# Kernel tuning notes

Hardware: AMD Instinct MI355X
Metric: run time of the kernel (lower is better)

The kernel has to match this reference:

```python
import jax, jax.numpy as jnp
import numpy as np

D_MODEL, N_STATE, L_MAX, BATCH = 256, 64, 4096, 8


def _hippo_pql(n):
    """NPLR-HiPPO decomposition: returns (lambda, p, q) in the eigenbasis (complex)."""
    i = np.arange(1, n + 1, dtype=np.float64)
    hippo = np.where(
        i[:, None] > i[None, :],
        np.sqrt(2 * i[:, None] + 1) * np.sqrt(2 * i[None, :] + 1),
        np.where(i[:, None] == i[None, :], i[:, None] + 1.0, 0.0),
    )
    p = 0.5 * np.sqrt(2 * i + 1.0)
    q = 2 * p
    S = -hippo + p[:, None] * q[None, :]  # normal matrix
    lam, V = np.linalg.eig(S)
    Vc = V.conj().T
    pc = Vc @ p.astype(np.complex128)
    qc = Vc @ q.astype(np.complex128)
    return lam.astype(np.complex64), pc.astype(np.complex64), qc.astype(np.complex64)


def setup_inputs() -> dict:
    key = jax.random.key(0)
    ks = jax.random.split(key, 6)
    lam, p, q = _hippo_pql(N_STATE)
    c2r = lambda z: jnp.asarray(np.stack([z.real, z.imag], axis=-1).astype(np.float32))
    xav = (2.0 / (D_MODEL + N_STATE)) ** 0.5  # xavier-normal std for [D, N]
    log_lo, log_hi = np.log(0.001), np.log(0.1)
    return {
        "u": jax.random.normal(ks[0], (BATCH, L_MAX, D_MODEL), jnp.float32),
        "B_ri": jax.random.normal(ks[1], (D_MODEL, N_STATE, 2), jnp.float32) * xav,
        "Ct_ri": jax.random.normal(ks[2], (D_MODEL, N_STATE, 2), jnp.float32) * xav,
        "lam_ri": c2r(lam),
        "p_ri": c2r(p),
        "q_ri": c2r(q),
        "log_step": jax.random.uniform(ks[3], (D_MODEL,), jnp.float32) * (log_hi - log_lo) + log_lo,
        "D_skip": jnp.ones((D_MODEL,), jnp.float32),
        "W": jax.random.normal(ks[4], (D_MODEL, D_MODEL), jnp.float32) / np.sqrt(D_MODEL),
        "b": jnp.zeros((D_MODEL,), jnp.float32),
        "gamma": jnp.ones((D_MODEL,), jnp.float32),
        "beta": jnp.zeros((D_MODEL,), jnp.float32),
    }


def _c(x):  # [..., 2] real -> complex
    return jax.lax.complex(x[..., 0], x[..., 1])


def _s4_kernel(lam_ri, p_ri, q_ri, B_ri, Ct_ri, log_step, L):
    """DPLR generating-function kernel (annotated-S4 / S4Torch math). Returns K [D, L]."""
    lam, p, q = _c(lam_ri), _c(p_ri), _c(q_ri)  # [N]
    B, Ct = _c(B_ri), _c(Ct_ri)                 # [D, N]
    step = jnp.exp(log_step)                    # [D]
    omega = jnp.exp(-2j * jnp.pi * jnp.arange(L) / L).astype(jnp.complex64)  # [L]
    g = (2.0 / step)[:, None] * ((1.0 - omega) / (1.0 + omega))[None, :]     # [D, L]
    c = 2.0 / (1.0 + omega)                                                  # [L]
    # shared Cauchy resolvent, computed once: [D, L, N]
    r = 1.0 / (g[:, :, None] - lam[None, None, :])
    k00 = jnp.einsum('dn,dln->dl', Ct.conj() * B, r)
    k01 = jnp.einsum('dn,dln->dl', Ct.conj() * p[None, :], r)
    k10 = jnp.einsum('dn,dln->dl', q.conj()[None, :] * B, r)
    k11 = jnp.einsum('n,dln->dl', q.conj() * p, r)
    at_roots = c[None, :] * (k00 - k01 * (1.0 / (1.0 + k11)) * k10)  # [D, L]
    return jnp.fft.ifft(at_roots, n=L, axis=-1).real                  # [D, L]


def reference(u, B_ri, Ct_ri, lam_ri, p_ri, q_ri, log_step, D_skip, W, b, gamma, beta):
    Bsz, L, Dm = u.shape
    K = _s4_kernel(lam_ri, p_ri, q_ri, B_ri, Ct_ri, log_step, L)  # [D, L]
    # non-circular convolution via length-2L FFT
    ud = jnp.fft.rfft(u, n=2 * L, axis=1)        # [B, L+1, D]
    Kd = jnp.fft.rfft(K, n=2 * L, axis=-1)       # [D, L+1]
    conv = jnp.fft.irfft(ud * Kd.T[None], n=2 * L, axis=1)[:, :L, :]
    z = conv + D_skip * u                        # S4Layer output
    z = jax.nn.gelu(z, approximate=False)        # nn.GELU (exact erf)
    z = z @ W.T + b                              # Linear(d, d); dropout p=0 -> identity
    x = z + u                                    # residual
    mu = x.mean(-1, keepdims=True)
    var = x.var(-1, keepdims=True)
    return gamma * (x - mu) * jax.lax.rsqrt(var + 1e-5) + beta  # LayerNorm
```

## Files before the change

### kernel.cpp

```cpp
#include <hip/hip_runtime.h>
#include <math.h>


typedef __attribute__((ext_vector_type(2))) float cf;
typedef __attribute__((ext_vector_type(8))) short bf16x8;
typedef __attribute__((ext_vector_type(4))) float f32x4;

__device__ __forceinline__ cf mkcf(float x, float y){ cf r; r.x = x; r.y = y; return r; }

__device__ __forceinline__ cf cadd(cf a, cf b){ return a + b; }
__device__ __forceinline__ cf csub(cf a, cf b){ return a - b; }
__device__ __forceinline__ cf cscale(cf a, float s){ return a * s; }
__device__ __forceinline__ cf cconj(cf a){ return mkcf(a.x, -a.y); }
__device__ __forceinline__ cf cmul(cf a, cf b){
  return mkcf(fmaf(a.x, b.x, -a.y*b.y), fmaf(a.x, b.y, a.y*b.x));
}
__device__ __forceinline__ void cmacc(cf& acc, cf a, cf b){
  acc.x = fmaf(a.x, b.x, fmaf(-a.y, b.y, acc.x));
  acc.y = fmaf(a.x, b.y, fmaf( a.y, b.x, acc.y));
}
__device__ __forceinline__ cf caddi(cf p, cf q){ return mkcf(p.x - q.y, p.y + q.x); }
__device__ __forceinline__ cf csubi(cf p, cf q){ return mkcf(p.x + q.y, p.y - q.x); }

__device__ __forceinline__ short f2bf(float x){
  union { float f; unsigned u; } v; v.f = x;
  unsigned r = v.u + 0x7fffu + ((v.u >> 16) & 1u);
  return (short)(r >> 16);
}

__device__ __forceinline__ constexpr int RI(int k){ return ((k & 3) << 2) | (k >> 2); }

#define C8 0.92387953251f
#define S8 0.38268343236f
#define RH 0.70710678119f

template<int DIR>
__device__ __forceinline__ void r4(cf& a, cf& b, cf& c, cf& d){
  cf T0 = a + c, T1 = a - c;
  cf T2 = b + d, Bd = b - d;
  a = T0 + T2; c = T0 - T2;
  if (DIR > 0){ b = caddi(T1, Bd); d = csubi(T1, Bd); }
  else        { b = csubi(T1, Bd); d = caddi(T1, Bd); }
}

template<int DIR, bool HZ>
__device__ __forceinline__ void fft16(cf* v){
  if constexpr (HZ){
    #pragma unroll
    for (int i = 0; i < 4; ++i){
      cf a = v[i], b = v[i+4];
      v[i]   = a + b;
      v[i+8] = a - b;
      if (DIR > 0){ v[i+4] = caddi(a, b); v[i+12] = csubi(a, b); }
      else        { v[i+4] = csubi(a, b); v[i+12] = caddi(a, b); }
    }
  } else {
    r4<DIR>(v[0], v[4], v[8],  v[12]);
    r4<DIR>(v[1], v[5], v[9],  v[13]);
    r4<DIR>(v[2], v[6], v[10], v[14]);
    r4<DIR>(v[3], v[7], v[11], v[15]);
  }
  constexpr float D = (float)DIR;
  const cf w1 = mkcf(C8,  D*S8);
  const cf w2 = mkcf(RH,  D*RH);
  const cf w3 = mkcf(S8,  D*C8);
  const cf w6 = mkcf(-RH, D*RH);
  const cf w9 = mkcf(-C8, -D*S8);
  v[5]  = cmul(v[5],  w1);
  v[6]  = cmul(v[6],  w2);
  v[7]  = cmul(v[7],  w3);
  v[9]  = cmul(v[9],  w2);
  v[10] = (DIR > 0) ? mkcf(-v[10].y, v[10].x) : mkcf(v[10].y, -v[10].x);
  v[11] = cmul(v[11], w6);
  v[13] = cmul(v[13], w3);
  v[14] = cmul(v[14], w6);
  v[15] = cmul(v[15], w9);
  r4<DIR>(v[0],  v[1],  v[2],  v[3]);
  r4<DIR>(v[4],  v[5],  v[6],  v[7]);
  r4<DIR>(v[8],  v[9],  v[10], v[11]);
  r4<DIR>(v[12], v[13], v[14], v[15]);
}

template<int DIR, bool HZ = false>
__device__ void fft4096_reg(cf* v, cf* lds){
  const int t = threadIdx.x;
  const int k1 = t >> 4, m2 = t & 15;
  const int swt = t ^ k1;
  constexpr float D = (float)DIR;
  fft16<DIR, HZ>(v);
  float sn, cs;
  __sincosf(D * 1.5339807878856412e-3f * (float)t, &sn, &cs);
  __syncthreads();
  {
    cf* p = lds + swt;
    cf w1 = mkcf(cs, sn);
    p[0]    = v[0];
    p[256]  = cmul(v[RI(1)],  w1);
    cf w2 = cmul(w1, w1);
    p[512]  = cmul(v[RI(2)],  w2);
    cf w3 = cmul(w2, w1);
    p[768]  = cmul(v[RI(3)],  w3);
    cf w4 = cmul(w2, w2);
    p[1024] = cmul(v[RI(4)],  w4);
    cf w5 = cmul(w4, w1);
    p[1280] = cmul(v[RI(5)],  w5);
    cf w6 = cmul(w4, w2);
    p[1536] = cmul(v[RI(6)],  w6);
    cf w7 = cmul(w4, w3);
    p[1792] = cmul(v[RI(7)],  w7);
    cf w8 = cmul(w4, w4);
    p[2048] = cmul(v[RI(8)],  w8);
    p[2304] = cmul(v[RI(9)],  cmul(w8, w1));
    p[2560] = cmul(v[RI(10)], cmul(w8, w2));
    p[2816] = cmul(v[RI(11)], cmul(w8, w3));
    p[3072] = cmul(v[RI(12)], cmul(w8, w4));
    p[3328] = cmul(v[RI(13)], cmul(w8, w5));
    p[3584] = cmul(v[RI(14)], cmul(w8, w6));
    p[3840] = cmul(v[RI(15)], cmul(w8, w7));
  }
  __syncthreads();
  {
    cf* p = lds + k1*256;
    #pragma unroll
    for (int m1 = 0; m1 < 16; ++m1) v[m1] = p[m1*16 + (m2 ^ m1)];
  }
  fft16<DIR, false>(v);
  __sincosf(D * 2.45436926061703e-2f * (float)m2, &sn, &cs);
  __syncthreads();
  {
    cf* p = lds + k1*256;
    cf w1 = mkcf(cs, sn);
    p[m2]              = v[0];
    p[16  + (m2^1)]    = cmul(v[RI(1)],  w1);
    cf w2 = cmul(w1, w1);
    p[32  + (m2^2)]    = cmul(v[RI(2)],  w2);
    cf w3 = cmul(w2, w1);
    p[48  + (m2^3)]    = cmul(v[RI(3)],  w3);
    cf w4 = cmul(w2, w2);
    p[64  + (m2^4)]    = cmul(v[RI(4)],  w4);
    cf w5 = cmul(w4, w1);
    p[80  + (m2^5)]    = cmul(v[RI(5)],  w5);
    cf w6 = cmul(w4, w2);
    p[96  + (m2^6)]    = cmul(v[RI(6)],  w6);
    cf w7 = cmul(w4, w3);
    p[112 + (m2^7)]    = cmul(v[RI(7)],  w7);
    cf w8 = cmul(w4, w4);
    p[128 + (m2^8)]    = cmul(v[RI(8)],  w8);
    p[144 + (m2^9)]    = cmul(v[RI(9)],  cmul(w8, w1));
    p[160 + (m2^10)]   = cmul(v[RI(10)], cmul(w8, w2));
    p[176 + (m2^11)]   = cmul(v[RI(11)], cmul(w8, w3));
    p[192 + (m2^12)]   = cmul(v[RI(12)], cmul(w8, w4));
    p[208 + (m2^13)]   = cmul(v[RI(13)], cmul(w8, w5));
    p[224 + (m2^14)]   = cmul(v[RI(14)], cmul(w8, w6));
    p[240 + (m2^15)]   = cmul(v[RI(15)], cmul(w8, w7));
  }
  __syncthreads();
  {
    const int ka = m2;
    cf* p = lds + k1*256 + ka*16;
    #pragma unroll
    for (int m2b = 0; m2b < 16; ++m2b) v[m2b] = p[m2b ^ ka];
  }
  fft16<DIR, false>(v);
}

__global__ __launch_bounds__(256)
void fused_head(const float* __restrict__ B_ri, const float* __restrict__ Ct_ri,
                const float* __restrict__ lam_ri, const float* __restrict__ p_ri,
                const float* __restrict__ q_ri, const float* __restrict__ log_step,
                float* __restrict__ KdE,
                const float* __restrict__ W, short* __restrict__ Wbf){
  __shared__ cf w00[64], w01[64], w10[64], w11[64], lamS[64];
  const int bid = blockIdx.x;
  const int tid = threadIdx.x;

  if (bid >= 2048){
    int t  = (bid - 2048) * 256 + tid;
    int o4 = t * 4;
    int j   = o4 & 7;
    int lm  = (o4 >> 3)  & 15;
    int lk  = (o4 >> 7)  & 3;
    int nt  = (o4 >> 9)  & 7;
    int fh2 = (o4 >> 12) & 1;
    int ks  = o4 >> 13;
    int f = fh2*128 + nt*16 + lm;
    int k = ks*32 + lk*8 + j;
    float4 wv = *(const float4*)(W + (size_t)f*256 + k);
    short4 o;
    o.x = f2bf(wv.x); o.y = f2bf(wv.y); o.z = f2bf(wv.z); o.w = f2bf(wv.w);
    *(short4*)(Wbf + o4) = o;
    return;
  }

  const int d     = bid >> 3;
  const int chunk = bid & 7;
  const float step = expf(log_step[d]);

  if (tid < 64){
    int n = tid;
    cf Bv = mkcf(B_ri[(d*64+n)*2],  B_ri[(d*64+n)*2+1]);
    cf Cv = mkcf(Ct_ri[(d*64+n)*2], Ct_ri[(d*64+n)*2+1]);
    cf pv = mkcf(p_ri[n*2], p_ri[n*2+1]);
    cf qv = mkcf(q_ri[n*2], q_ri[n*2+1]);
    lamS[n] = mkcf(lam_ri[n*2], lam_ri[n*2+1]);
    cf Cc = cconj(Cv), qc = cconj(qv);
    w00[n] = cmul(Cc, Bv);
    w01[n] = cmul(Cc, pv);
    w10[n] = cmul(qc, Bv);
    w11[n] = cmul(qc, pv);
  }
  __syncthreads();

  cf* out = (cf*)KdE + (size_t)d * 2049;
  const int l = chunk * 256 + tid;
  {
    float th = -(6.28318530717958647692f * (float)l) * (1.0f/4096.0f);
    float sn, cs; __sincosf(th, &sn, &cs);
    cf opw = mkcf(1.0f + cs,  sn);
    cf omw = mkcf(1.0f - cs, -sn);
    float idn = __builtin_amdgcn_rcpf(fmaf(opw.x, opw.x, opw.y*opw.y));
    cf ratio = mkcf((omw.x*opw.x + omw.y*opw.y)*idn,
                    (omw.y*opw.x - omw.x*opw.y)*idn);
    cf g  = cscale(ratio, 2.0f / step);
    cf cc = mkcf(2.0f*opw.x*idn, -2.0f*opw.y*idn);
    cf k00 = mkcf(0,0), k01 = mkcf(0,0), k10 = mkcf(0,0), k11 = mkcf(0,0);
    #pragma unroll 4
    for (int n = 0; n < 64; ++n){
      cf den = g - lamS[n];
      float is = __builtin_amdgcn_rcpf(fmaf(den.x, den.x, den.y*den.y));
      cf r = mkcf(den.x*is, -den.y*is);
      cmacc(k00, w00[n], r);
      cmacc(k01, w01[n], r);
      cmacc(k10, w10[n], r);
      cmacc(k11, w11[n], r);
    }
    cf onep = mkcf(1.0f + k11.x, k11.y);
    float ii = __builtin_amdgcn_rcpf(fmaf(onep.x, onep.x, onep.y*onep.y));
    cf inv1p = mkcf(onep.x*ii, -onep.y*ii);
    cf corr = cmul(k01, cmul(k10, inv1p));
    out[l] = cmul(cc, csub(k00, corr));
  }
  if (chunk == 7 && tid == 255){
    cf s00 = mkcf(0.f, 0.f);
    for (int n = 0; n < 64; ++n) s00 = cadd(s00, w00[n]);
    out[2048] = cscale(s00, 0.5f * step);
  }
}

__device__ void fft_kd_body(int d, cf* L, const float* __restrict__ KdE,
                            float* __restrict__ KdO){
  const int t = threadIdx.x;
  const cf* kdE = (const cf*)KdE + (size_t)d * 2049;
  cf* kdO = (cf*)KdO + (size_t)d * 2048;
  cf v[16];
  const float inv = 1.0f / 4096.0f;
  #pragma unroll
  for (int n1 = 0; n1 < 16; ++n1){
    int m = n1*256 + t;
    cf a = (m <= 2048) ? kdE[m] : cconj(kdE[4096 - m]);
    v[n1] = cscale(a, inv);
  }
  fft4096_reg<+1>(v, L);
  const int k1 = t >> 4, ka = t & 15;
  const int xb = (k1 ^ ka) + 16*ka;
  const int swt = t ^ k1;
  __syncthreads();
  #pragma unroll
  for (int kb = 0; kb < 16; ++kb){
    int g = k1 + 16*ka + 256*kb;
    float kr = v[RI(kb)].x;
    float sn, cs; __sincosf(-7.669903939428206e-4f * (float)g, &sn, &cs);
    L[xb + 256*kb] = mkcf(kr*cs, kr*sn);
  }
  __syncthreads();
  #pragma unroll
  for (int n1 = 0; n1 < 16; ++n1) v[n1] = L[swt + n1*256];
  fft4096_reg<-1>(v, L);
  #pragma unroll
  for (int kb = 0; kb < 8; ++kb)
    kdO[k1 + 16*ka + 256*kb] = v[RI(kb)];
}

__global__ __launch_bounds__(256)
void fused_mid(const float* __restrict__ KdE, float* __restrict__ KdO,
               const float* __restrict__ u, float* __restrict__ ut){
  __shared__ cf L[4096];
  const int bid = blockIdx.x;
  if (bid < 256){
    fft_kd_body(bid, L, KdE, KdO);
    return;
  }
  float (*tile)[33] = (float(*)[33])L;
  const int m  = bid - 256;
  const int l0 = (m & 127) * 32;
  const int d0 = ((m >> 7) & 7) * 32;
  const int b  = m >> 10;
  const int tx = threadIdx.x & 31;
  const int ty = threadIdx.x >> 5;
  const float* ub = u + (size_t)b * 4096 * 256;
  #pragma unroll
  for (int it = 0; it < 4; ++it){
    int l = l0 + ty + it*8;
    tile[tx][ty + it*8] = ub[(size_t)l*256 + d0 + tx];
  }
  __syncthreads();
  float* utb = ut + (size_t)b * 256 * 4096;
  #pragma unroll
  for (int it = 0; it < 4; ++it){
    int dd = d0 + ty + it*8;
    utb[(size_t)dd*4096 + l0 + tx] = tile[ty + it*8][tx];
  }
}

__device__ __forceinline__ float gelu_exact(float x){
  float z = fabsf(x) * 0.70710678118654752f;
  float tt = __builtin_amdgcn_rcpf(fmaf(0.3275911f, z, 1.0f));
  float poly = fmaf(fmaf(fmaf(fmaf(1.061405429f, tt, -1.453152027f), tt,
                    1.421413741f), tt, -0.284496736f), tt, 0.254829592f) * tt;
  float ec = poly * __expf(-z*z);
  float phi = (x >= 0.f) ? fmaf(-0.5f, ec, 1.0f) : 0.5f * ec;
  return x * phi;
}

__global__ __launch_bounds__(256)
void s4_conv(float* __restrict__ ut, const float* __restrict__ KdE,
             const float* __restrict__ KdO, const float* __restrict__ Dsk){
  __shared__ cf L[4096];
  const int row = blockIdx.x;
  const int d   = row & 255;
  const int t   = threadIdx.x;
  cf* rp = (cf*)(ut + (size_t)row * 4096);
  const float dskd = Dsk[d];

  cf v[16], uin[8];
  #pragma unroll
  for (int n1 = 0; n1 < 8; ++n1){ uin[n1] = rp[n1*256 + t]; v[n1] = uin[n1]; }
  #pragma unroll
  for (int n1 = 8; n1 < 16; ++n1) v[n1] = mkcf(0.f, 0.f);

  fft4096_reg<-1, true>(v, L);
  const int k1 = t >> 4, ka = t & 15;
  const int xb  = (k1 ^ ka) + 16*ka;
  const int swt = t ^ k1;
  const int t2  = 256 - t;
  const int swt2 = t2 ^ ((t2 >> 4) & 15);
  __syncthreads();
  #pragma unroll
  for (int kb = 0; kb < 16; ++kb)
    L[xb + 256*kb] = v[RI(kb)];
  __syncthreads();

  const cf* kdE = (const cf*)KdE + (size_t)d * 2049;
  const cf* kdO = (const cf*)KdO + (size_t)d * 2048;
  #pragma unroll
  for (int m = 0; m < 8; ++m){
    int k = t + m*256;
    if (k == 0){
      cf z0 = L[0];
      float U0 = z0.x + z0.y, UN = z0.x - z0.y;
      cf P0 = cscale(kdE[0], U0);
      cf PN = cscale(kdE[2048], UN);
      cf cPN = cconj(PN);
      cf Ep = cscale(cadd(P0, cPN), 0.5f);
      cf Op = cscale(csub(P0, cPN), 0.5f);
      L[0] = mkcf(Ep.x - Op.y, Ep.y + Op.x);
      cf P = cmul(cconj(L[2048]), kdE[1024]);
      L[2048] = cconj(P);
    } else {
      cf zk = L[swt + m*256];
      cf zj = L[(15 - m)*256 + swt2];
      int h = k >> 1;
      cf kk, kj;
      if (k & 1){ kk = kdO[h]; kj = kdO[2047 - h]; }
      else      { kk = kdE[h]; kj = kdE[2048 - h]; }
      float sn, cs; __sincosf(7.669903939428206e-4f * (float)k, &sn, &cs);
      cf KS = mkcf(0.5f*(kk.x + kj.x), 0.5f*(kk.y - kj.y));
      cf KD = mkcf(0.5f*(kk.x - kj.x), 0.5f*(kk.y + kj.y));
      cf KA  = KS - KD * sn;
      cf KAp = KS + KD * sn;
      cf KB  = mkcf(-cs * KD.y, cs * KD.x);
      cf Ak, Aj;
      Ak.x = fmaf(KA.x, zk.x, fmaf(-KA.y, zk.y, fmaf(KB.x, zj.x,  KB.y*zj.y)));
      Ak.y = fmaf(KA.x, zk.y, fmaf( KA.y, zk.x, fmaf(KB.y, zj.x, -KB.x*zj.y)));
      Aj.x = fmaf( KAp.x, zj.x, fmaf(KAp.y, zj.y, fmaf(-KB.x, zk.x, KB.y*zk.y)));
      Aj.y = fmaf(-KAp.y, zj.x, fmaf(KAp.x, zj.y, fmaf( KB.x, zk.y, KB.y*zk.x)));
      L[swt + m*256] = Ak;
      L[(15 - m)*256 + swt2] = Aj;
    }
  }
  __syncthreads();

  #pragma unroll
  for (int n1 = 0; n1 < 16; ++n1) v[n1] = L[swt + n1*256];
  fft4096_reg<+1>(v, L);

  __syncthreads();
  #pragma unroll
  for (int kb = 0; kb < 8; ++kb)
    L[xb + 256*kb] = v[RI(kb)];
  __syncthreads();
  const float inv = 1.0f / 4096.0f;
  unsigned* og = (unsigned*)rp;
  #pragma unroll
  for (int n1 = 0; n1 < 8; ++n1){
    cf cv = L[swt + n1*256];
    float x0 = fmaf(dskd, uin[n1].x, cv.x * inv);
    float x1 = fmaf(dskd, uin[n1].y, cv.y * inv);
    unsigned b0 = (unsigned)(unsigned short)f2bf(gelu_exact(x0));
    unsigned b1 = (unsigned)(unsigned short)f2bf(gelu_exact(x1));
    og[n1*256 + t] = b0 | (b1 << 16);
  }
}

__global__ __launch_bounds__(256)
void mfma_gemm_ln(const float* __restrict__ utg, const short* __restrict__ Wbf,
                  const float* __restrict__ bias, const float* __restrict__ u,
                  const float* __restrict__ gamma, const float* __restrict__ beta,
                  float* __restrict__ out){
  __shared__ short St[64][32];
  __shared__ float prm[2][256];
  __shared__ float2 red[2][2][16];
  const int w    = threadIdx.x >> 6;
  const int l    = threadIdx.x & 63;
  const int lm   = l & 15;
  const int lk   = l >> 4;
  const int tokB = blockIdx.x * 32;
  const int b    = tokB >> 12;
  const int l0   = tokB & 4095;

  prm[0][threadIdx.x] = gamma[threadIdx.x];
  prm[1][threadIdx.x] = beta[threadIdx.x];

  const int srow = l >> 2;
  const int tg   = l & 3;
  const char* ubase = (const char*)utg + (size_t)(b * 256) * 16384;
  bf16x8 pre[4];
  #pragma unroll
  for (int c = 0; c < 4; ++c){
    int r = c*64 + w*16 + srow;
    pre[c] = *(const bf16x8*)((const unsigned short*)(ubase + (size_t)r * 16384) + l0 + tg*8);
  }

  const int th = (w & 1) * 16;
  const int fh2 = w >> 1;
  const int fh = fh2 * 128;
  const int tt = tokB + th + lm;
  const float* ur = u + (size_t)tt * 256 + fh;
  const float* br = bias + fh;
  f32x4 acc[8];
  #pragma unroll
  for (int nt = 0; nt < 8; ++nt){
    const float4 uv = *(const float4*)(ur + nt*16 + lk*4);
    const float4 bv = *(const float4*)(br + nt*16 + lk*4);
    acc[nt] = (f32x4){uv.x + bv.x, uv.y + bv.y, uv.z + bv.z, uv.w + bv.w};
  }

  const int tg_tok = (th + lm) >> 3;
  const int tlo    = lm & 7;

  #pragma unroll
  for (int c = 0; c < 4; ++c){
    __syncthreads();
    {
      int r  = w*16 + srow;
      int sl = (tg ^ ((r >> 3) & 3)) * 8;
      *(bf16x8*)&St[r][sl] = pre[c];
    }
    __syncthreads();
    #pragma unroll
    for (int s2 = 0; s2 < 2; ++s2){
      const int ks  = c*2 + s2;
      const int idx = ((tg_tok ^ lk) << 3) | tlo;
      bf16x8 zf;
      #pragma unroll
      for (int j = 0; j < 8; ++j)
        zf[j] = St[s2*32 + lk*8 + j][idx];
      const short* wbase = Wbf + (size_t)(ks*2 + fh2)*4096 + lk*128 + lm*8;
      #pragma unroll
      for (int nt = 0; nt < 8; ++nt){
        const bf16x8* ap = (const bf16x8*)(wbase + nt*512);
        acc[nt] = __builtin_amdgcn_mfma_f32_16x16x32_bf16(*ap, zf, acc[nt], 0, 0, 0);
      }
    }
  }

  float s = 0.f, s2 = 0.f;
  #pragma unroll
  for (int nt = 0; nt < 8; ++nt){
    s += acc[nt][0] + acc[nt][1] + acc[nt][2] + acc[nt][3];
    s2 = fmaf(acc[nt][0], acc[nt][0], s2);
    s2 = fmaf(acc[nt][1], acc[nt][1], s2);
    s2 = fmaf(acc[nt][2], acc[nt][2], s2);
    s2 = fmaf(acc[nt][3], acc[nt][3], s2);
  }
  s  += __shfl_xor(s,  16); s  += __shfl_xor(s,  32);
  s2 += __shfl_xor(s2, 16); s2 += __shfl_xor(s2, 32);
  __syncthreads();
  if (lk == 0) red[w & 1][fh2][lm] = make_float2(s, s2);
  __syncthreads();
  const float2 pj = red[w & 1][fh2 ^ 1][lm];
  const float st = s + pj.x, s2t = s2 + pj.y;
  const float mu = st * (1.0f/256.0f);
  const float rs = rsqrtf(s2t * (1.0f/256.0f) - mu*mu + 1e-5f);
  float* orow = out + (size_t)tt * 256 + fh;
  #pragma unroll
  for (int nt = 0; nt < 8; ++nt){
    const int f0 = fh + nt*16 + lk*4;
    const float4 gv = *(const float4*)&prm[0][f0];
    const float4 ev = *(const float4*)&prm[1][f0];
    float4 o;
    o.x = (acc[nt][0] - mu) * rs * gv.x + ev.x;
    o.y = (acc[nt][1] - mu) * rs * gv.y + ev.y;
    o.z = (acc[nt][2] - mu) * rs * gv.z + ev.z;
    o.w = (acc[nt][3] - mu) * rs * gv.w + ev.w;
    *(float4*)(orow + nt*16 + lk*4) = o;
  }
}

extern "C" void kernel_launch(void* const* d_in, const int* in_sizes, int n_in,
                              void* d_out, int out_size, void* d_ws, size_t ws_size,
                              hipStream_t stream){
  (void)in_sizes; (void)n_in; (void)out_size; (void)ws_size;
  const float* u        = (const float*)d_in[0];
  const float* B_ri     = (const float*)d_in[1];
  const float* Ct_ri    = (const float*)d_in[2];
  const float* lam_ri   = (const float*)d_in[3];
  const float* p_ri     = (const float*)d_in[4];
  const float* q_ri     = (const float*)d_in[5];
  const float* log_step = (const float*)d_in[6];
  const float* D_skip   = (const float*)d_in[7];
  const float* W        = (const float*)d_in[8];
  const float* bias     = (const float*)d_in[9];
  const float* gamma    = (const float*)d_in[10];
  const float* beta     = (const float*)d_in[11];
  float* out = (float*)d_out;

  char* ws = (char*)d_ws;
  float* KdE = (float*)(ws);
  float* KdO = (float*)(ws + 4196352);
  short* Wbf = (short*)(ws + 4196352 + 4194304);
  float* ut  = (float*)(ws + 4196352 + 4194304 + 131072);

  fused_head  <<<2112, 256, 0, stream>>>(B_ri, Ct_ri, lam_ri, p_ri, q_ri,
                                         log_step, KdE, W, Wbf);
  fused_mid   <<<8448, 256, 0, stream>>>(KdE, KdO, u, ut);
  s4_conv     <<<2048, 256, 0, stream>>>(ut, KdE, KdO, D_skip);
  mfma_gemm_ln<<<1024, 256, 0, stream>>>(ut, Wbf, bias, u, gamma, beta, out);
}
```

Before: 103.1 us.

## Prefetch kernel spectrum before FFT, double-buffer GEMM staging, cap conv occupancy

```diff
diff --git a/kernel.cpp b/kernel.cpp
--- a/kernel.cpp
+++ b/kernel.cpp
@@ -19,8 +19,6 @@
   acc.x = fmaf(a.x, b.x, fmaf(-a.y, b.y, acc.x));
   acc.y = fmaf(a.x, b.y, fmaf( a.y, b.x, acc.y));
 }
-__device__ __forceinline__ cf caddi(cf p, cf q){ return mkcf(p.x - q.y, p.y + q.x); }
-__device__ __forceinline__ cf csubi(cf p, cf q){ return mkcf(p.x + q.y, p.y - q.x); }
 
 __device__ __forceinline__ short f2bf(float x){
   union { float f; unsigned u; } v; v.f = x;
@@ -39,8 +37,8 @@
   cf T0 = a + c, T1 = a - c;
   cf T2 = b + d, Bd = b - d;
   a = T0 + T2; c = T0 - T2;
-  if (DIR > 0){ b = caddi(T1, Bd); d = csubi(T1, Bd); }
-  else        { b = csubi(T1, Bd); d = caddi(T1, Bd); }
+  cf iBd = (DIR > 0) ? mkcf(-Bd.y, Bd.x) : mkcf(Bd.y, -Bd.x);
+  b = T1 + iBd; d = T1 - iBd;
 }
 
 template<int DIR, bool HZ>
@@ -49,10 +47,11 @@
     #pragma unroll
     for (int i = 0; i < 4; ++i){
       cf a = v[i], b = v[i+4];
-      v[i]   = a + b;
-      v[i+8] = a - b;
-      if (DIR > 0){ v[i+4] = caddi(a, b); v[i+12] = csubi(a, b); }
-      else        { v[i+4] = csubi(a, b); v[i+12] = caddi(a, b); }
+      cf ib = (DIR > 0) ? mkcf(-b.y, b.x) : mkcf(b.y, -b.x);
+      v[i]    = a + b;
+      v[i+8]  = a - b;
+      v[i+4]  = a + ib;
+      v[i+12] = a - ib;
     }
   } else {
     r4<DIR>(v[0], v[4], v[8],  v[12]);
@@ -322,7 +321,7 @@
   return x * phi;
 }
 
-__global__ __launch_bounds__(256)
+__global__ __launch_bounds__(256, 5)
 void s4_conv(float* __restrict__ ut, const float* __restrict__ KdE,
              const float* __restrict__ KdO, const float* __restrict__ Dsk){
   __shared__ cf L[4096];
@@ -332,11 +331,21 @@
   cf* rp = (cf*)(ut + (size_t)row * 4096);
   const float dskd = Dsk[d];
 
-  cf v[16], uin[8];
+  const cf* kdE = (const cf*)KdE + (size_t)d * 2049;
+  const cf* kdO = (const cf*)KdO + (size_t)d * 2048;
+
+  cf v[16], uin[8], kkv[8], kjv[8];
   #pragma unroll
   for (int n1 = 0; n1 < 8; ++n1){ uin[n1] = rp[n1*256 + t]; v[n1] = uin[n1]; }
   #pragma unroll
   for (int n1 = 8; n1 < 16; ++n1) v[n1] = mkcf(0.f, 0.f);
+  #pragma unroll
+  for (int m = 0; m < 8; ++m){
+    int k = t + m*256;
+    int h = k >> 1;
+    if (k & 1){ kkv[m] = kdO[h]; kjv[m] = kdO[2047 - h]; }
+    else      { kkv[m] = kdE[h]; kjv[m] = kdE[2048 - h]; }
+  }
 
   fft4096_reg<-1, true>(v, L);
   const int k1 = t >> 4, ka = t & 15;
@@ -350,16 +359,14 @@
     L[xb + 256*kb] = v[RI(kb)];
   __syncthreads();
 
-  const cf* kdE = (const cf*)KdE + (size_t)d * 2049;
-  const cf* kdO = (const cf*)KdO + (size_t)d * 2048;
   #pragma unroll
   for (int m = 0; m < 8; ++m){
     int k = t + m*256;
     if (k == 0){
       cf z0 = L[0];
       float U0 = z0.x + z0.y, UN = z0.x - z0.y;
-      cf P0 = cscale(kdE[0], U0);
-      cf PN = cscale(kdE[2048], UN);
+      cf P0 = cscale(kkv[0], U0);
+      cf PN = cscale(kjv[0], UN);
       cf cPN = cconj(PN);
       cf Ep = cscale(cadd(P0, cPN), 0.5f);
       cf Op = cscale(csub(P0, cPN), 0.5f);
@@ -369,10 +376,7 @@
     } else {
       cf zk = L[swt + m*256];
       cf zj = L[(15 - m)*256 + swt2];
-      int h = k >> 1;
-      cf kk, kj;
-      if (k & 1){ kk = kdO[h]; kj = kdO[2047 - h]; }
-      else      { kk = kdE[h]; kj = kdE[2048 - h]; }
+      cf kk = kkv[m], kj = kjv[m];
       float sn, cs; __sincosf(7.669903939428206e-4f * (float)k, &sn, &cs);
       cf KS = mkcf(0.5f*(kk.x + kj.x), 0.5f*(kk.y - kj.y));
       cf KD = mkcf(0.5f*(kk.x - kj.x), 0.5f*(kk.y + kj.y));
@@ -417,7 +421,7 @@
                   const float* __restrict__ bias, const float* __restrict__ u,
                   const float* __restrict__ gamma, const float* __restrict__ beta,
                   float* __restrict__ out){
-  __shared__ short St[64][32];
+  __shared__ short St[2][64][32];
   __shared__ float prm[2][256];
   __shared__ float2 red[2][2][16];
   const int w    = threadIdx.x >> 6;
@@ -460,11 +464,11 @@
 
   #pragma unroll
   for (int c = 0; c < 4; ++c){
-    __syncthreads();
+    const int buf = c & 1;
     {
       int r  = w*16 + srow;
       int sl = (tg ^ ((r >> 3) & 3)) * 8;
-      *(bf16x8*)&St[r][sl] = pre[c];
+      *(bf16x8*)&St[buf][r][sl] = pre[c];
     }
     __syncthreads();
     #pragma unroll
@@ -474,7 +478,7 @@
       bf16x8 zf;
       #pragma unroll
       for (int j = 0; j < 8; ++j)
-        zf[j] = St[s2*32 + lk*8 + j][idx];
+        zf[j] = St[buf][s2*32 + lk*8 + j][idx];
       const short* wbase = Wbf + (size_t)(ks*2 + fh2)*4096 + lk*128 + lm*8;
       #pragma unroll
       for (int nt = 0; nt < 8; ++nt){
```

Measured after the change: 120.5 us. +16.9%, slower.
